# Kernel tuning notes

Hardware: AMD Instinct MI355X
Metric: run time of the kernel (lower is better)

The kernel has to match this reference:

```python
import jax, jax.numpy as jnp
import numpy as np

B, S, D, H, E, K = 4, 2048, 1024, 4096, 8, 2
CAP_RATIO = 1.05


def setup_inputs() -> dict:
    key = jax.random.key(0)
    k0, k1, k2, k3 = jax.random.split(key, 4)
    x = jax.random.normal(k0, (B, S, D), jnp.float32)
    # router gating weight (xavier-uniform-ish scale)
    Wg = jax.random.normal(k1, (E, D), jnp.float32) * np.float32(np.sqrt(2.0 / (D + E)))
    W1 = jax.random.normal(k2, (E, D, H), jnp.float32) * np.float32(0.02)
    b1 = jnp.zeros((E, H), jnp.float32)
    W2 = jax.random.normal(k3, (E, H, D), jnp.float32) * np.float32(0.02)
    b2 = jnp.zeros((E, D), jnp.float32)
    return {"x": x, "Wg": Wg, "W1": W1, "b1": b1, "W2": W2, "b2": b2}


def reference(x, Wg, W1, b1, W2, b2):
    Bs, Ss, Dd = x.shape
    T = Bs * Ss
    C = int(round(K * T * CAP_RATIO / E))  # static buffer capacity per expert
    xf = x.reshape(T, Dd)

    # --- router (eval mode: no noise) ---
    logits = xf @ Wg.T                       # (T, E)
    gates = jax.nn.softmax(logits, axis=-1)  # (T, E)
    topv, topi = jax.lax.top_k(gates, K)     # (T, K)

    # --- capacity-limited dispatch: FCFS over slot-major (slot, token) order ---
    idx_sm = topi.T.reshape(-1)                              # (K*T,) slot-major expert ids
    oh = jax.nn.one_hot(idx_sm, E, dtype=jnp.int32)          # (K*T, E)
    pos_sm = (jnp.cumsum(oh, axis=0) * oh).sum(-1) - 1       # 0-based rank within expert
    within_sm = pos_sm < C
    pos_sm = jnp.where(within_sm, pos_sm, C)                 # C == out-of-bounds sentinel
    pos = pos_sm.reshape(K, T).T                             # (T, K)
    within = within_sm.reshape(K, T).T                       # (T, K) bool

    # --- combine weights: mask dropped slots, renormalize over active slots ---
    w = topv * within.astype(topv.dtype)
    sums = w.sum(-1, keepdims=True)
    w = jnp.where(sums > 0, w / sums, w)

    # --- scatter tokens into per-expert capacity buffers ---
    e_flat = topi.reshape(-1)                                # (T*K,)
    pos_flat = pos.reshape(-1)                               # (T*K,)
    x_ts = jnp.broadcast_to(xf[:, None, :], (T, K, Dd)).reshape(T * K, Dd)
    expert_in = jnp.zeros((E, C, Dd), x.dtype).at[e_flat, pos_flat].set(x_ts, mode='drop')

    # --- per-expert MLP (grouped GEMM) ---
    h = jax.nn.gelu(jnp.einsum('ecd,edh->ech', expert_in, W1) + b1[:, None, :], approximate=False)
    o = jnp.einsum('ech,ehd->ecd', h, W2) + b2[:, None, :]   # (E, C, D)

    # --- gather back and weighted combine (dropped slots gather 0) ---
    y_ts = o.at[e_flat, pos_flat].get(mode='fill', fill_value=0).reshape(T, K, Dd)
    y = jnp.einsum('tk,tkd->td', w, y_ts)                    # (T, D)

    # --- auxiliary losses ---
    imp = gates.sum(0)                                       # (E,)
    l_imp = (jnp.std(imp) / (imp.mean() + 1e-6)) ** 2
    tpe = (oh * within_sm[:, None].astype(jnp.int32)).sum(0).astype(jnp.float32)
    l_load = (jnp.std(tpe) / (tpe.mean() + 1e-6)) ** 2
    l_aux = 0.5 * (l_imp + l_load)

    return y.reshape(Bs, Ss, Dd), l_aux, l_load
```

## Files before the change

kernel.cpp:

```cpp
#include <hip/hip_runtime.h>
#include <math.h>

typedef short short8v __attribute__((ext_vector_type(8)));
typedef float f32x4 __attribute__((ext_vector_type(4)));
typedef unsigned short ushort4v __attribute__((ext_vector_type(4)));

#define T_TOK 8192
#define DDIM 1024
#define HDIM 4096
#define NE 8
#define CCAP 2150
#define CPAD 2304

__device__ __forceinline__ unsigned short f2bf(float f) {
  union { float f; unsigned u; } a; a.f = f;
  unsigned r = a.u + 0x7fffu + ((a.u >> 16) & 1u);
  return (unsigned short)(r >> 16);
}
__device__ __forceinline__ float bf2f(unsigned short h) {
  union { unsigned u; float f; } a; a.u = ((unsigned)h) << 16;
  return a.f;
}

#define GLOAD_LDS16(gp, lp)                                                   \
  __builtin_amdgcn_global_load_lds(                                           \
      (const __attribute__((address_space(1))) void*)(gp),                    \
      (__attribute__((address_space(3))) void*)(lp), 16, 0, 0)

#define BAR()                                   \
  do {                                          \
    asm volatile("" ::: "memory");              \
    __builtin_amdgcn_s_barrier();               \
    asm volatile("" ::: "memory");              \
  } while (0)

__global__ __launch_bounds__(256) void router_kernel(
    const float* __restrict__ x, const float* __restrict__ Wg,
    int2* __restrict__ topi, float2* __restrict__ topv,
    float* __restrict__ blkimp) {
  __shared__ float wg[NE * DDIM];
  __shared__ float gsh[4][NE];
  int tid = threadIdx.x;
  for (int i = tid; i < NE * DDIM / 4; i += 256)
    ((float4*)wg)[i] = ((const float4*)Wg)[i];
  __syncthreads();
  int w = tid >> 6, lane = tid & 63;
  int t = blockIdx.x * 4 + w;
  const float* xr = x + (size_t)t * DDIM;
  float p[NE] = {0.f, 0.f, 0.f, 0.f, 0.f, 0.f, 0.f, 0.f};
#pragma unroll
  for (int j = 0; j < 16; ++j) {
    float xv = xr[lane + 64 * j];
#pragma unroll
    for (int e = 0; e < NE; ++e)
      p[e] = fmaf(xv, wg[e * DDIM + lane + 64 * j], p[e]);
  }
#pragma unroll
  for (int e = 0; e < NE; ++e) {
#pragma unroll
    for (int off = 32; off > 0; off >>= 1) p[e] += __shfl_xor(p[e], off, 64);
  }
  float mx = p[0];
#pragma unroll
  for (int e = 1; e < NE; ++e) mx = fmaxf(mx, p[e]);
  float g[NE];
  float s = 0.f;
#pragma unroll
  for (int e = 0; e < NE; ++e) { g[e] = expf(p[e] - mx); s += g[e]; }
  float inv = 1.0f / s;
#pragma unroll
  for (int e = 0; e < NE; ++e) g[e] *= inv;
  int i0 = 0; float v0 = g[0];
#pragma unroll
  for (int e = 1; e < NE; ++e) if (g[e] > v0) { v0 = g[e]; i0 = e; }
  int i1 = -1; float v1 = -1.0f;
#pragma unroll
  for (int e = 0; e < NE; ++e)
    if (e != i0 && g[e] > v1) { v1 = g[e]; i1 = e; }
  if (lane == 0) {
    topi[t] = make_int2(i0, i1);
    topv[t] = make_float2(v0, v1);
#pragma unroll
    for (int e = 0; e < NE; ++e) gsh[w][e] = g[e];
  }
  __syncthreads();
  if (tid < NE)
    blkimp[blockIdx.x * NE + tid] =
        gsh[0][tid] + gsh[1][tid] + gsh[2][tid] + gsh[3][tid];
}

__global__ __launch_bounds__(256) void dispatch_kernel(
    const int2* __restrict__ topi, const float2* __restrict__ topv,
    const float* __restrict__ blkimp, int2* __restrict__ posmj,
    float2* __restrict__ wmaj, float* __restrict__ tail) {
  __shared__ unsigned char eid[2 * T_TOK];
  __shared__ unsigned short possm[2 * T_TOK];
  __shared__ int cnt_sh[NE];
  __shared__ float part[32][NE];
  int tid = threadIdx.x;
  for (int i = tid; i < T_TOK; i += 256) {
    int2 ti = topi[i];
    eid[i] = (unsigned char)ti.x;
    eid[T_TOK + i] = (unsigned char)ti.y;
  }
  __syncthreads();
  if (tid < 64) {
    int lane = tid;
    unsigned long long low = (1ull << lane) - 1ull;
    int c0 = 0, c1 = 0, c2 = 0, c3 = 0, c4 = 0, c5 = 0, c6 = 0, c7 = 0;
    for (int base = 0; base < 2 * T_TOK; base += 64) {
      int e = eid[base + lane];
      unsigned long long m0 = __ballot(e == 0);
      unsigned long long m1 = __ballot(e == 1);
      unsigned long long m2 = __ballot(e == 2);
      unsigned long long m3 = __ballot(e == 3);
      unsigned long long m4 = __ballot(e == 4);
      unsigned long long m5 = __ballot(e == 5);
      unsigned long long m6 = __ballot(e == 6);
      unsigned long long m7 = __ballot(e == 7);
      int rank = 0;
      if (e == 0) rank = c0 + __popcll(m0 & low);
      if (e == 1) rank = c1 + __popcll(m1 & low);
      if (e == 2) rank = c2 + __popcll(m2 & low);
      if (e == 3) rank = c3 + __popcll(m3 & low);
      if (e == 4) rank = c4 + __popcll(m4 & low);
      if (e == 5) rank = c5 + __popcll(m5 & low);
      if (e == 6) rank = c6 + __popcll(m6 & low);
      if (e == 7) rank = c7 + __popcll(m7 & low);
      possm[base + lane] = (unsigned short)((rank < CCAP) ? rank : CCAP);
      c0 += __popcll(m0); c1 += __popcll(m1); c2 += __popcll(m2);
      c3 += __popcll(m3); c4 += __popcll(m4); c5 += __popcll(m5);
      c6 += __popcll(m6); c7 += __popcll(m7);
    }
    if (lane == 0) {
      cnt_sh[0] = c0; cnt_sh[1] = c1; cnt_sh[2] = c2; cnt_sh[3] = c3;
      cnt_sh[4] = c4; cnt_sh[5] = c5; cnt_sh[6] = c6; cnt_sh[7] = c7;
    }
  }
  __syncthreads();
  for (int t = tid; t < T_TOK; t += 256) {
    int p0 = possm[t], p1 = possm[T_TOK + t];
    float2 tv = topv[t];
    float w0 = (p0 < CCAP) ? tv.x : 0.0f;
    float w1 = (p1 < CCAP) ? tv.y : 0.0f;
    float s = w0 + w1;
    if (s > 0.0f) { w0 /= s; w1 /= s; }
    posmj[t] = make_int2(p0, p1);
    wmaj[t] = make_float2(w0, w1);
  }
  {
    int sl = tid >> 3, e8 = tid & 7;
    float s = 0.f;
    for (int b = sl; b < 2048; b += 32) s += blkimp[b * NE + e8];
    part[sl][e8] = s;
  }
  __syncthreads();
  if (tid == 0) {
    float imp[NE], te[NE];
    for (int e = 0; e < NE; ++e) {
      float s = 0.f;
      for (int j = 0; j < 32; ++j) s += part[j][e];
      imp[e] = s;
      int c = cnt_sh[e];
      te[e] = (float)(c < CCAP ? c : CCAP);
    }
    float mi = 0.f, mt = 0.f;
    for (int e = 0; e < NE; ++e) { mi += imp[e]; mt += te[e]; }
    mi *= 0.125f; mt *= 0.125f;
    float vi = 0.f, vt = 0.f;
    for (int e = 0; e < NE; ++e) {
      vi += (imp[e] - mi) * (imp[e] - mi);
      vt += (te[e] - mt) * (te[e] - mt);
    }
    vi *= 0.125f; vt *= 0.125f;
    float ai = sqrtf(vi) / (mi + 1e-6f);
    float at = sqrtf(vt) / (mt + 1e-6f);
    tail[0] = 0.5f * (ai * ai + at * at);
    tail[1] = at * at;
  }
}

__global__ __launch_bounds__(256) void scatter_kernel(
    const float* __restrict__ x, const int2* __restrict__ topi,
    const int2* __restrict__ posmj, unsigned short* __restrict__ ein) {
  int tid = threadIdx.x;
  int gid = blockIdx.x * 4 + (tid >> 6);
  int lane = tid & 63;
  int t = gid >> 1, k = gid & 1;
  int2 pp = posmj[t];
  int p = k ? pp.y : pp.x;
  if (p >= CCAP) return;
  int2 ii = topi[t];
  int e = k ? ii.y : ii.x;
  const float4* src = (const float4*)(x + (size_t)t * DDIM);
  unsigned short* dst = ein + ((size_t)e * CPAD + p) * DDIM;
#pragma unroll
  for (int j = 0; j < 4; ++j) {
    int c = j * 64 + lane;
    float4 v = src[c];
    ushort4v o;
    o.x = f2bf(v.x); o.y = f2bf(v.y); o.z = f2bf(v.z); o.w = f2bf(v.w);
    *(ushort4v*)(dst + (size_t)c * 4) = o;
  }
}

__global__ __launch_bounds__(256) void transpose_cvt_kernel(
    const float* __restrict__ W, unsigned short* __restrict__ WT, int R,
    int Cc) {
  __shared__ unsigned short tile[64][72];
  int rt = R >> 6, ct = Cc >> 6;
  int per_e = rt * ct;
  int e = blockIdx.x / per_e;
  int rem = blockIdx.x % per_e;
  int tr = rem % rt, tc = rem / rt;
  int r0 = tr << 6, c0 = tc << 6;
  const float* We = W + (size_t)e * R * Cc;
  unsigned short* WTe = WT + (size_t)e * R * Cc;
  int tid = threadIdx.x;
  {
    int rl = tid >> 2, cb = (tid & 3) << 4;
    const float* src = We + (size_t)(r0 + rl) * Cc + c0 + cb;
#pragma unroll
    for (int j = 0; j < 16; j += 4) {
      float4 v = *(const float4*)(src + j);
      tile[rl][cb + j + 0] = f2bf(v.x);
      tile[rl][cb + j + 1] = f2bf(v.y);
      tile[rl][cb + j + 2] = f2bf(v.z);
      tile[rl][cb + j + 3] = f2bf(v.w);
    }
  }
  __syncthreads();
  {
    int cl = tid >> 2, rb = (tid & 3) << 4;
    unsigned short* dst = WTe + (size_t)(c0 + cl) * R + r0 + rb;
#pragma unroll
    for (int j = 0; j < 16; j += 4) {
      ushort4v o;
      o.x = tile[rb + j + 0][cl];
      o.y = tile[rb + j + 1][cl];
      o.z = tile[rb + j + 2][cl];
      o.w = tile[rb + j + 3][cl];
      *(ushort4v*)(dst + j) = o;
    }
  }
}

template <bool GELU>
__global__ __launch_bounds__(512, 2) void gemm256_kernel(
    const unsigned short* __restrict__ A, const unsigned short* __restrict__ B,
    const float* __restrict__ bias, unsigned short* __restrict__ Out0,
    unsigned short* __restrict__ Out1, int M, int N, int Kz, int Ksub, int NT,
    int mt, int nt) {
  __shared__ __align__(16) char smem[131072];
  int nwg = gridDim.x;
  int bid = blockIdx.x;
  int swz = (bid & 7) * (nwg >> 3) + (bid >> 3);
  int bm = swz % mt;
  int r = swz / mt;
  int bn = r % nt;
  int r2 = r / nt;
  int e = r2 & 7;
  int ks = r2 >> 3;
  unsigned short* Outp = ks ? Out1 : Out0;
  int koff = ks * Ksub;

  int tid = threadIdx.x;
  int w = tid >> 6, lane = tid & 63;
  int wm = w >> 2, wn = w & 3;
  int fr = lane & 15, g = lane >> 4;
  size_t Kzs = (size_t)Kz;
  const unsigned short* Ae = A + ((size_t)e * M + (size_t)bm * 256) * Kzs + koff;
  const unsigned short* Be = B + ((size_t)e * N + (size_t)bn * 256) * Kzs + koff;

  auto stage = [&](const unsigned short* gb, int buf, int isB, int kh) {
#pragma unroll
    for (int j = 0; j < 2; ++j) {
      const unsigned short* src =
          gb + (size_t)((j * 8 + w) * 16 + fr) * Kzs + kh * 32 + g * 8;
      char* dst = smem + (isB << 16) + (buf << 15) + (kh << 14) +
                  ((j * 8 + w) << 10) + lane * 16;
      GLOAD_LDS16(src, dst);
    }
  };
  auto lda = [&](int buf, int kk, int m16) -> short8v {
    return *(const short8v*)(smem + (buf << 15) + (kk << 14) + (m16 << 10) +
                             lane * 16);
  };
  auto ldb = [&](int buf, int kk, int n16) -> short8v {
    return *(const short8v*)(smem + 65536 + (buf << 15) + (kk << 14) +
                             (n16 << 10) + lane * 16);
  };

  f32x4 acc[8][4] = {};

  stage(Ae, 0, 0, 0); stage(Be, 0, 1, 0);
  stage(Ae, 0, 0, 1); stage(Be, 0, 1, 1);
  stage(Ae + 64, 1, 0, 0); stage(Be + 64, 1, 1, 0);
  asm volatile("s_waitcnt vmcnt(4)" ::: "memory");
  BAR();

  for (int t = 0; t < NT; ++t) {
    int c = t & 1;
    const unsigned short* An1 = Ae + (size_t)(t + 1) * 64;
    const unsigned short* Bn1 = Be + (size_t)(t + 1) * 64;
    const unsigned short* An2 = Ae + (size_t)(t + 2) * 64;
    const unsigned short* Bn2 = Be + (size_t)(t + 2) * 64;
    short8v Bk[4], Af[4];
#pragma unroll
    for (int n = 0; n < 4; ++n) Bk[n] = ldb(c, 0, wn * 4 + n);
#pragma unroll
    for (int m = 0; m < 4; ++m) Af[m] = lda(c, 0, wm * 8 + m);
    if (t + 1 < NT) stage(An1, c ^ 1, 0, 1);
    BAR();
    __builtin_amdgcn_s_setprio(1);
#pragma unroll
    for (int m = 0; m < 4; ++m)
#pragma unroll
      for (int n = 0; n < 4; ++n)
        acc[m][n] = __builtin_amdgcn_mfma_f32_16x16x32_bf16(Af[m], Bk[n],
                                                            acc[m][n], 0, 0, 0);
    __builtin_amdgcn_s_setprio(0);
    BAR();
#pragma unroll
    for (int m = 0; m < 4; ++m) Af[m] = lda(c, 0, wm * 8 + 4 + m);
    if (t + 1 < NT) stage(Bn1, c ^ 1, 1, 1);
    BAR();
    __builtin_amdgcn_s_setprio(1);
#pragma unroll
    for (int m = 0; m < 4; ++m)
#pragma unroll
      for (int n = 0; n < 4; ++n)
        acc[4 + m][n] = __builtin_amdgcn_mfma_f32_16x16x32_bf16(
            Af[m], Bk[n], acc[4 + m][n], 0, 0, 0);
    __builtin_amdgcn_s_setprio(0);
    BAR();
#pragma unroll
    for (int n = 0; n < 4; ++n) Bk[n] = ldb(c, 1, wn * 4 + n);
#pragma unroll
    for (int m = 0; m < 4; ++m) Af[m] = lda(c, 1, wm * 8 + m);
    if (t + 2 < NT) stage(An2, c, 0, 0);
    BAR();
    __builtin_amdgcn_s_setprio(1);
#pragma unroll
    for (int m = 0; m < 4; ++m)
#pragma unroll
      for (int n = 0; n < 4; ++n)
        acc[m][n] = __builtin_amdgcn_mfma_f32_16x16x32_bf16(Af[m], Bk[n],
                                                            acc[m][n], 0, 0, 0);
    __builtin_amdgcn_s_setprio(0);
    BAR();
#pragma unroll
    for (int m = 0; m < 4; ++m) Af[m] = lda(c, 1, wm * 8 + 4 + m);
    if (t + 2 < NT) {
      stage(Bn2, c, 1, 0);
      asm volatile("s_waitcnt vmcnt(4)" ::: "memory");
    } else {
      asm volatile("s_waitcnt vmcnt(0)" ::: "memory");
    }
    BAR();
    __builtin_amdgcn_s_setprio(1);
#pragma unroll
    for (int m = 0; m < 4; ++m)
#pragma unroll
      for (int n = 0; n < 4; ++n)
        acc[4 + m][n] = __builtin_amdgcn_mfma_f32_16x16x32_bf16(
            Af[m], Bk[n], acc[4 + m][n], 0, 0, 0);
    __builtin_amdgcn_s_setprio(0);
    BAR();
  }

  float bv[4];
#pragma unroll
  for (int n = 0; n < 4; ++n)
    bv[n] = (ks == 0)
                ? bias[(size_t)e * N + (size_t)bn * 256 + wn * 64 + n * 16 + fr]
                : 0.0f;
  char* wreg = smem + w * 16384;
#pragma unroll
  for (int m = 0; m < 8; ++m)
#pragma unroll
    for (int n = 0; n < 4; ++n)
#pragma unroll
      for (int j = 0; j < 4; ++j) {
        float v = acc[m][n][j] + bv[n];
        if (GELU) v = 0.5f * v * (1.0f + erff(v * 0.70710678118654752f));
        int rl = m * 16 + g * 4 + j;
        *(unsigned short*)(wreg + rl * 128 + (n * 16 + fr) * 2) = f2bf(v);
      }
  unsigned short* Oe = Outp +
                       ((size_t)e * M + (size_t)bm * 256 + (size_t)wm * 128) * N +
                       (size_t)bn * 256 + (size_t)wn * 64;
#pragma unroll
  for (int pass = 0; pass < 16; ++pass) {
    int rr = pass * 8 + (lane >> 3);
    int ch = lane & 7;
    short8v vv = *(const short8v*)(wreg + rr * 128 + ch * 16);
    *(short8v*)(Oe + (size_t)rr * N + ch * 8) = vv;
  }
}

__global__ __launch_bounds__(256) void gather_kernel(
    const unsigned short* __restrict__ obufA,
    const unsigned short* __restrict__ obufB, const int2* __restrict__ topi,
    const int2* __restrict__ posmj, const float2* __restrict__ wmaj,
    float* __restrict__ y) {
  int tid = threadIdx.x;
  int w = tid >> 6, lane = tid & 63;
  int t = blockIdx.x * 4 + w;
  int2 pp = posmj[t];
  int2 ii = topi[t];
  float2 ww = wmaj[t];
  float* yr = y + (size_t)t * DDIM;
  size_t o0 = ((size_t)ii.x * CPAD + pp.x) * DDIM;
  size_t o1 = ((size_t)ii.y * CPAD + pp.y) * DDIM;
  bool v0 = pp.x < CCAP, v1 = pp.y < CCAP;
#pragma unroll
  for (int j = 0; j < 4; ++j) {
    int c = j * 64 + lane;
    float ax = 0.f, ay = 0.f, az = 0.f, aw = 0.f;
    if (v0) {
      ushort4v a = *(const ushort4v*)(obufA + o0 + (size_t)c * 4);
      ushort4v b = *(const ushort4v*)(obufB + o0 + (size_t)c * 4);
      ax += ww.x * (bf2f(a.x) + bf2f(b.x));
      ay += ww.x * (bf2f(a.y) + bf2f(b.y));
      az += ww.x * (bf2f(a.z) + bf2f(b.z));
      aw += ww.x * (bf2f(a.w) + bf2f(b.w));
    }
    if (v1) {
      ushort4v a = *(const ushort4v*)(obufA + o1 + (size_t)c * 4);
      ushort4v b = *(const ushort4v*)(obufB + o1 + (size_t)c * 4);
      ax += ww.y * (bf2f(a.x) + bf2f(b.x));
      ay += ww.y * (bf2f(a.y) + bf2f(b.y));
      az += ww.y * (bf2f(a.z) + bf2f(b.z));
      aw += ww.y * (bf2f(a.w) + bf2f(b.w));
    }
    ((float4*)yr)[c] = make_float4(ax, ay, az, aw);
  }
}

extern "C" void kernel_launch(void* const* d_in, const int* in_sizes, int n_in,
                              void* d_out, int out_size, void* d_ws,
                              size_t ws_size, hipStream_t stream) {
  (void)in_sizes; (void)n_in; (void)out_size; (void)ws_size;
  const float* x = (const float*)d_in[0];
  const float* Wg = (const float*)d_in[1];
  const float* W1 = (const float*)d_in[2];
  const float* b1 = (const float*)d_in[3];
  const float* W2 = (const float*)d_in[4];
  const float* b2 = (const float*)d_in[5];
  float* out = (float*)d_out;

  char* ws = (char*)d_ws;
  size_t off = 0;
  auto alloc = [&](size_t b) {
    char* p = ws + off;
    off += (b + 255) & ~(size_t)255;
    return p;
  };
  unsigned short* ein = (unsigned short*)alloc((size_t)NE * CPAD * DDIM * 2);
  unsigned short* hbuf = (unsigned short*)alloc((size_t)NE * CPAD * HDIM * 2);
  unsigned short* obuf = (unsigned short*)alloc((size_t)NE * CPAD * DDIM * 2);
  unsigned short* w1t = (unsigned short*)alloc((size_t)NE * HDIM * DDIM * 2);
  unsigned short* w2t = (unsigned short*)alloc((size_t)NE * DDIM * HDIM * 2);
  int2* topi = (int2*)alloc(T_TOK * sizeof(int2));
  float2* topv = (float2*)alloc(T_TOK * sizeof(float2));
  int2* posmj = (int2*)alloc(T_TOK * sizeof(int2));
  float2* wmaj = (float2*)alloc(T_TOK * sizeof(float2));
  float* blkimp = (float*)alloc(2048 * NE * sizeof(float));

  transpose_cvt_kernel<<<NE * (DDIM / 64) * (HDIM / 64), 256, 0, stream>>>(
      W1, w1t, DDIM, HDIM);
  transpose_cvt_kernel<<<NE * (HDIM / 64) * (DDIM / 64), 256, 0, stream>>>(
      W2, w2t, HDIM, DDIM);
  router_kernel<<<T_TOK / 4, 256, 0, stream>>>(x, Wg, topi, topv, blkimp);
  dispatch_kernel<<<1, 256, 0, stream>>>(topi, topv, blkimp, posmj, wmaj,
                                         out + (size_t)T_TOK * DDIM);
  scatter_kernel<<<(2 * T_TOK) / 4, 256, 0, stream>>>(x, topi, posmj, ein);

  gemm256_kernel<true><<<NE * 9 * 16, 512, 0, stream>>>(
      ein, w1t, b1, hbuf, hbuf, CPAD, HDIM, DDIM, DDIM, DDIM / 64, 9, 16);
  gemm256_kernel<false><<<NE * 9 * 4 * 2, 512, 0, stream>>>(
      hbuf, w2t, b2, obuf, ein, CPAD, DDIM, HDIM, HDIM / 2, HDIM / 128, 9, 4);

  gather_kernel<<<T_TOK / 4, 256, 0, stream>>>(obuf, ein, topi, posmj, wmaj,
                                               out);
}
```

Measured before the change: 683.3 us.

## Double-buffer MFMA register fragments to prefetch LDS reads ahead of compute

Restructures the GEMM main loop so A/B fragments are read from LDS one phase ahead into separate register sets (a0/a1, b0/b1). LDS reads then overlap the previous MFMA block instead of stalling right before it, and the vmcnt waits are retuned to match. Staging address arithmetic is also precomputed into byte offsets, which removes per-call multiplies. The extra fragment registers raise VGPR pressure, and the changed waitcnt/barrier ordering risks races if the counts are wrong.

Result: no change. 680.9 us (-0.4%).

```diff
diff --git a/kernel.cpp b/kernel.cpp
--- a/kernel.cpp
+++ b/kernel.cpp
@@ -269,18 +269,18 @@
   int wm = w >> 2, wn = w & 3;
   int fr = lane & 15, g = lane >> 4;
   size_t Kzs = (size_t)Kz;
-  const unsigned short* Ae = A + ((size_t)e * M + (size_t)bm * 256) * Kzs + koff;
-  const unsigned short* Be = B + ((size_t)e * N + (size_t)bn * 256) * Kzs + koff;
-
-  auto stage = [&](const unsigned short* gb, int buf, int isB, int kh) {
-#pragma unroll
-    for (int j = 0; j < 2; ++j) {
-      const unsigned short* src =
-          gb + (size_t)((j * 8 + w) * 16 + fr) * Kzs + kh * 32 + g * 8;
-      char* dst = smem + (isB << 16) + (buf << 15) + (kh << 14) +
-                  ((j * 8 + w) << 10) + lane * 16;
-      GLOAD_LDS16(src, dst);
-    }
+  const char* Ab = (const char*)(A + ((size_t)e * M + (size_t)bm * 256) * Kzs + koff);
+  const char* Bb = (const char*)(B + ((size_t)e * N + (size_t)bn * 256) * Kzs + koff);
+
+  size_t ro0 = (size_t)(w * 16 + fr) * Kzs * 2 + (size_t)g * 16;
+  size_t ro1 = ro0 + (size_t)128 * Kzs * 2;
+  int ld0 = (w << 10) + lane * 16;
+  int ld1 = ((8 + w) << 10) + lane * 16;
+
+  auto stage = [&](const char* gb, int buf, int isB, int kh) {
+    int base = (isB << 16) + (buf << 15) + (kh << 14);
+    GLOAD_LDS16(gb + ro0 + kh * 64, smem + base + ld0);
+    GLOAD_LDS16(gb + ro1 + kh * 64, smem + base + ld1);
   };
   auto lda = [&](int buf, int kk, int m16) -> short8v {
     return *(const short8v*)(smem + (buf << 15) + (kk << 14) + (m16 << 10) +
@@ -292,38 +292,47 @@
   };
 
   f32x4 acc[8][4] = {};
-
-  stage(Ae, 0, 0, 0); stage(Be, 0, 1, 0);
-  stage(Ae, 0, 0, 1); stage(Be, 0, 1, 1);
-  stage(Ae + 64, 1, 0, 0); stage(Be + 64, 1, 1, 0);
-  asm volatile("s_waitcnt vmcnt(4)" ::: "memory");
+  short8v a0[4], a1[4], b0[4], b1[4];
+
+  stage(Ab, 0, 0, 0); stage(Bb, 0, 1, 0);
+  stage(Ab, 0, 0, 1); stage(Bb, 0, 1, 1);
+  stage(Ab + 128, 1, 0, 0); stage(Bb + 128, 1, 1, 0);
+  asm volatile("s_waitcnt vmcnt(8)" ::: "memory");
   BAR();
+#pragma unroll
+  for (int m = 0; m < 4; ++m) a0[m] = lda(0, 0, wm * 8 + m);
+#pragma unroll
+  for (int n = 0; n < 4; ++n) b0[n] = ldb(0, 0, wn * 4 + n);
 
   for (int t = 0; t < NT; ++t) {
-    int c = t & 1;
-    const unsigned short* An1 = Ae + (size_t)(t + 1) * 64;
-    const unsigned short* Bn1 = Be + (size_t)(t + 1) * 64;
-    const unsigned short* An2 = Ae + (size_t)(t + 2) * 64;
-    const unsigned short* Bn2 = Be + (size_t)(t + 2) * 64;
-    short8v Bk[4], Af[4];
-#pragma unroll
-    for (int n = 0; n < 4; ++n) Bk[n] = ldb(c, 0, wn * 4 + n);
-#pragma unroll
-    for (int m = 0; m < 4; ++m) Af[m] = lda(c, 0, wm * 8 + m);
-    if (t + 1 < NT) stage(An1, c ^ 1, 0, 1);
+    int c = t & 1, cn = c ^ 1;
+    const char* At1 = Ab + (size_t)(t + 1) * 128;
+    const char* Bt1 = Bb + (size_t)(t + 1) * 128;
+    const char* At2 = Ab + (size_t)(t + 2) * 128;
+    const char* Bt2 = Bb + (size_t)(t + 2) * 128;
+#pragma unroll
+    for (int m = 0; m < 4; ++m) a1[m] = lda(c, 0, wm * 8 + 4 + m);
+    if (t + 1 < NT) stage(At1, cn, 0, 1);
     BAR();
     __builtin_amdgcn_s_setprio(1);
 #pragma unroll
     for (int m = 0; m < 4; ++m)
 #pragma unroll
       for (int n = 0; n < 4; ++n)
-        acc[m][n] = __builtin_amdgcn_mfma_f32_16x16x32_bf16(Af[m], Bk[n],
+        acc[m][n] = __builtin_amdgcn_mfma_f32_16x16x32_bf16(a0[m], b0[n],
                                                             acc[m][n], 0, 0, 0);
     __builtin_amdgcn_s_setprio(0);
-    BAR();
-#pragma unroll
-    for (int m = 0; m < 4; ++m) Af[m] = lda(c, 0, wm * 8 + 4 + m);
-    if (t + 1 < NT) stage(Bn1, c ^ 1, 1, 1);
+    if (t + 1 < NT) {
+      asm volatile("s_waitcnt vmcnt(6)" ::: "memory");
+    } else {
+      asm volatile("s_waitcnt vmcnt(0)" ::: "memory");
+    }
+    BAR();
+#pragma unroll
+    for (int m = 0; m < 4; ++m) a0[m] = lda(c, 1, wm * 8 + m);
+#pragma unroll
+    for (int n = 0; n < 4; ++n) b1[n] = ldb(c, 1, wn * 4 + n);
+    if (t + 1 < NT) stage(Bt1, cn, 1, 1);
     BAR();
     __builtin_amdgcn_s_setprio(1);
 #pragma unroll
@@ -331,40 +340,44 @@
 #pragma unroll
       for (int n = 0; n < 4; ++n)
         acc[4 + m][n] = __builtin_amdgcn_mfma_f32_16x16x32_bf16(
-            Af[m], Bk[n], acc[4 + m][n], 0, 0, 0);
+            a1[m], b0[n], acc[4 + m][n], 0, 0, 0);
     __builtin_amdgcn_s_setprio(0);
     BAR();
 #pragma unroll
-    for (int n = 0; n < 4; ++n) Bk[n] = ldb(c, 1, wn * 4 + n);
-#pragma unroll
-    for (int m = 0; m < 4; ++m) Af[m] = lda(c, 1, wm * 8 + m);
-    if (t + 2 < NT) stage(An2, c, 0, 0);
+    for (int m = 0; m < 4; ++m) a1[m] = lda(c, 1, wm * 8 + 4 + m);
+    if (t + 2 < NT) stage(At2, c, 0, 0);
     BAR();
     __builtin_amdgcn_s_setprio(1);
 #pragma unroll
     for (int m = 0; m < 4; ++m)
 #pragma unroll
       for (int n = 0; n < 4; ++n)
-        acc[m][n] = __builtin_amdgcn_mfma_f32_16x16x32_bf16(Af[m], Bk[n],
+        acc[m][n] = __builtin_amdgcn_mfma_f32_16x16x32_bf16(a0[m], b1[n],
                                                             acc[m][n], 0, 0, 0);
     __builtin_amdgcn_s_setprio(0);
     BAR();
-#pragma unroll
-    for (int m = 0; m < 4; ++m) Af[m] = lda(c, 1, wm * 8 + 4 + m);
     if (t + 2 < NT) {
-      stage(Bn2, c, 1, 0);
+      stage(Bt2, c, 1, 0);
+      asm volatile("s_waitcnt vmcnt(8)" ::: "memory");
+    } else if (t + 1 < NT) {
       asm volatile("s_waitcnt vmcnt(4)" ::: "memory");
     } else {
       asm volatile("s_waitcnt vmcnt(0)" ::: "memory");
     }
     BAR();
+    if (t + 1 < NT) {
+#pragma unroll
+      for (int m = 0; m < 4; ++m) a0[m] = lda(cn, 0, wm * 8 + m);
+#pragma unroll
+      for (int n = 0; n < 4; ++n) b0[n] = ldb(cn, 0, wn * 4 + n);
+    }
     __builtin_amdgcn_s_setprio(1);
 #pragma unroll
     for (int m = 0; m < 4; ++m)
 #pragma unroll
       for (int n = 0; n < 4; ++n)
         acc[4 + m][n] = __builtin_amdgcn_mfma_f32_16x16x32_bf16(
-            Af[m], Bk[n], acc[4 + m][n], 0, 0, 0);
+            a1[m], b1[n], acc[4 + m][n], 0, 0, 0);
     __builtin_amdgcn_s_setprio(0);
     BAR();
   }
```
